# Kernel tuning notes

Hardware: AMD Instinct MI355X
Metric: run time of the kernel (lower is better)

Reference implementation:

```python
import jax, jax.numpy as jnp
import numpy as np

N_NODES = 10000
N_EDGES = 320000
F_IN = 128
HID = 32


def sage_mean(x, src, dst, W_self, W_neigh, b, n_nodes):
    # mean aggregation over in-neighbors (messages flow src -> dst)
    msg = x[src]                                   # [E, F]
    agg = jax.ops.segment_sum(msg, dst, num_segments=n_nodes)   # [N, F]
    deg = jax.ops.segment_sum(jnp.ones((src.shape[0],), x.dtype), dst,
                              num_segments=n_nodes)             # [N]
    h_neigh = agg / jnp.maximum(deg, 1.0)[:, None]
    return x @ W_self + h_neigh @ W_neigh + b


def setup_inputs() -> dict:
    key = jax.random.key(0)
    ks = jax.random.split(key, 12)
    s = 0.05
    return {
        "n_feats": jax.random.normal(ks[0], (N_NODES, F_IN), jnp.float32),
        "src": jax.random.randint(ks[1], (N_EDGES,), 0, N_NODES, jnp.int32),
        "dst": jax.random.randint(ks[2], (N_EDGES,), 0, N_NODES, jnp.int32),
        "eps": jax.random.normal(ks[3], (N_NODES, HID), jnp.float32),
        "W1_self": jax.random.normal(ks[4], (F_IN, HID), jnp.float32) * s,
        "W1_neigh": jax.random.normal(ks[5], (F_IN, HID), jnp.float32) * s,
        "b1": jnp.zeros((HID,), jnp.float32),
        "Wmu_self": jax.random.normal(ks[6], (HID, HID), jnp.float32) * s,
        "Wmu_neigh": jax.random.normal(ks[7], (HID, HID), jnp.float32) * s,
        "bmu": jnp.zeros((HID,), jnp.float32),
        "Wls_self": jax.random.normal(ks[8], (HID, HID), jnp.float32) * s,
        "Wls_neigh": jax.random.normal(ks[9], (HID, HID), jnp.float32) * s,
        "bls": jnp.zeros((HID,), jnp.float32),
    }


def reference(n_feats, src, dst, eps, W1_self, W1_neigh, b1,
              Wmu_self, Wmu_neigh, bmu, Wls_self, Wls_neigh, bls):
    n = n_feats.shape[0]
    h = jax.nn.relu(sage_mean(n_feats, src, dst, W1_self, W1_neigh, b1, n))
    mu = sage_mean(h, src, dst, Wmu_self, Wmu_neigh, bmu, n)
    logstd = sage_mean(h, src, dst, Wls_self, Wls_neigh, bls, n)
    z = mu + eps * jnp.exp(logstd)          # reparameterize
    adj = jax.nn.sigmoid(z @ z.T)           # dot-product decode, [N, N]
    return adj, mu, logstd
```

## Files before the change

kernel.cpp:

```cpp
#include <hip/hip_runtime.h>
#include <hip/hip_bf16.h>


#define N_NODES 10000
#define N_EDGES 320000
#define F_IN 128
#define HID 32

__global__ __launch_bounds__(256) void k_gemm_in(
    const float* __restrict__ x, const float* __restrict__ Ws,
    const float* __restrict__ Wn, const float* __restrict__ b,
    float* __restrict__ outS, float* __restrict__ outN) {
  __shared__ float sWs[F_IN * HID];
  __shared__ float sWn[F_IN * HID];
  __shared__ float sx[32 * F_IN];
  const int t = threadIdx.x;
  const int node0 = blockIdx.x * 32;
  #pragma unroll
  for (int i = t * 4; i < F_IN * HID; i += 1024) {
    *(float4*)&sWs[i] = *(const float4*)&Ws[i];
    *(float4*)&sWn[i] = *(const float4*)&Wn[i];
  }
  #pragma unroll
  for (int i = t * 4; i < 32 * F_IN; i += 1024) {
    const int r = i >> 7, k = i & 127;
    const int gr = node0 + r;
    float4 v = make_float4(0.f, 0.f, 0.f, 0.f);
    if (gr < N_NODES) v = *(const float4*)&x[gr * F_IN + k];
    *(float4*)&sx[i] = v;
  }
  __syncthreads();
  const int c = t & 31, g = t >> 5;
  float accS[4] = {0.f, 0.f, 0.f, 0.f};
  float accN[4] = {0.f, 0.f, 0.f, 0.f};
  #pragma unroll 4
  for (int k = 0; k < F_IN; ++k) {
    const float ws = sWs[k * HID + c];
    const float wn = sWn[k * HID + c];
    #pragma unroll
    for (int m = 0; m < 4; ++m) {
      const float a = sx[(g + 8 * m) * F_IN + k];
      accS[m] += a * ws;
      accN[m] += a * wn;
    }
  }
  const float bc = b[c];
  #pragma unroll
  for (int m = 0; m < 4; ++m) {
    const int node = node0 + g + 8 * m;
    if (node < N_NODES) {
      outS[node * HID + c] = accS[m] + bc;
      outN[node * HID + c] = accN[m];
    }
  }
}

__global__ __launch_bounds__(256) void k_aggregate(
    const float* __restrict__ feat, const int* __restrict__ src,
    const int* __restrict__ dst, float* __restrict__ agg,
    float* __restrict__ deg) {
  const int tid = blockIdx.x * 256 + threadIdx.x;
  const int e = tid >> 5;
  const int k = tid & 31;
  if (e >= N_EDGES) return;
  const int s = src[e];
  const int d = dst[e];
  atomicAdd(&agg[d * HID + k], feat[s * HID + k]);
  if (deg != nullptr && k == 0) atomicAdd(&deg[d], 1.0f);
}

__global__ __launch_bounds__(256) void k_layer1_finish(
    const float* __restrict__ xws, const float* __restrict__ agg,
    const float* __restrict__ deg, float* __restrict__ h) {
  const int i = blockIdx.x * 256 + threadIdx.x;
  if (i >= N_NODES * HID) return;
  const int node = i >> 5;
  float dv = deg[node];
  dv = dv > 1.f ? dv : 1.f;
  const float v = xws[i] + agg[i] / dv;
  h[i] = v > 0.f ? v : 0.f;
}

__global__ __launch_bounds__(256) void k_layer2(
    const float* __restrict__ h, const float* __restrict__ aggh,
    const float* __restrict__ deg, const float* __restrict__ eps,
    const float* __restrict__ Wms, const float* __restrict__ Wmn,
    const float* __restrict__ bm, const float* __restrict__ Wls,
    const float* __restrict__ Wln, const float* __restrict__ bl,
    float* __restrict__ mu_out, float* __restrict__ ls_out,
    float* __restrict__ z) {
  __shared__ float sMs[HID * HID], sMn[HID * HID];
  __shared__ float sLs[HID * HID], sLn[HID * HID];
  __shared__ float sh[8 * HID], shn[8 * HID];
  const int t = threadIdx.x;
  {
    const int i = t * 4;
    *(float4*)&sMs[i] = *(const float4*)&Wms[i];
    *(float4*)&sMn[i] = *(const float4*)&Wmn[i];
    *(float4*)&sLs[i] = *(const float4*)&Wls[i];
    *(float4*)&sLn[i] = *(const float4*)&Wln[i];
  }
  const int node0 = blockIdx.x * 8;
  const int lr = t >> 5;
  const int gnode_ld = node0 + lr;
  if (gnode_ld < N_NODES) {
    float dv = deg[gnode_ld];
    dv = dv > 1.f ? dv : 1.f;
    sh[t] = h[node0 * HID + t];
    shn[t] = aggh[node0 * HID + t] / dv;
  } else {
    sh[t] = 0.f;
    shn[t] = 0.f;
  }
  __syncthreads();
  const int r = t >> 5, c = t & 31;
  const int node = node0 + r;
  float mu = 0.f, ls = 0.f;
  #pragma unroll 8
  for (int k = 0; k < HID; ++k) {
    const float a = sh[r * HID + k];
    const float an = shn[r * HID + k];
    mu += a * sMs[k * HID + c] + an * sMn[k * HID + c];
    ls += a * sLs[k * HID + c] + an * sLn[k * HID + c];
  }
  if (node < N_NODES) {
    mu += bm[c];
    ls += bl[c];
    const int idx = node * HID + c;
    mu_out[idx] = mu;
    ls_out[idx] = ls;
    z[idx] = mu + eps[idx] * __expf(ls);
  }
}

#define NT_COL 157
#define NWG (NT_COL * NT_COL)
#define NWG_Q (NWG / 8)
#define NWG_R (NWG % 8)
__global__ __launch_bounds__(256, 4) void k_decode(const float* __restrict__ z,
                                                   float* __restrict__ adj) {
  __shared__ float za[64][36];
  __shared__ float zb[64][36];
  const int bid = blockIdx.x;
  const int xcd = bid & 7, idx = bid >> 3;
  const int wg = (xcd < NWG_R) ? xcd * (NWG_Q + 1) + idx
                               : NWG_R * (NWG_Q + 1) + (xcd - NWG_R) * NWG_Q + idx;
  const int rowt = wg / NT_COL, colt = wg % NT_COL;
  const int r0 = rowt * 64;
  const int c0 = colt * 64;
  const int t = threadIdx.x;
  #pragma unroll
  for (int i = t; i < 512; i += 256) {
    const int row = i >> 3, k4 = (i & 7) << 2;
    const int gr = r0 + row;
    const int gc = c0 + row;
    float4 va = make_float4(0.f, 0.f, 0.f, 0.f);
    float4 vb = make_float4(0.f, 0.f, 0.f, 0.f);
    if (gr < N_NODES) va = *(const float4*)&z[gr * HID + k4];
    if (gc < N_NODES) vb = *(const float4*)&z[gc * HID + k4];
    *(float4*)&za[row][k4] = va;
    *(float4*)&zb[row][k4] = vb;
  }
  __syncthreads();
  const int tx = t & 15, ty = t >> 4;
  float acc[4][4];
  #pragma unroll
  for (int i = 0; i < 4; ++i)
    #pragma unroll
    for (int j = 0; j < 4; ++j) acc[i][j] = 0.f;

  #pragma unroll 4
  for (int k = 0; k < HID; ++k) {
    float a[4], b[4];
    #pragma unroll
    for (int i = 0; i < 4; ++i) a[i] = za[ty + i * 16][k];
    #pragma unroll
    for (int j = 0; j < 4; ++j) b[j] = zb[tx + j * 16][k];
    #pragma unroll
    for (int i = 0; i < 4; ++i)
      #pragma unroll
      for (int j = 0; j < 4; ++j) acc[i][j] += a[i] * b[j];
  }

  #pragma unroll
  for (int i = 0; i < 4; ++i) {
    const int r = r0 + ty + i * 16;
    if (r >= N_NODES) continue;
    float* rowp = adj + (size_t)r * N_NODES;
    #pragma unroll
    for (int j = 0; j < 4; ++j) {
      const int c = c0 + tx + j * 16;
      if (c < N_NODES) {
        const float v = acc[i][j];
        rowp[c] = __builtin_amdgcn_rcpf(1.f + __expf(-v));
      }
    }
  }
}

extern "C" void kernel_launch(void* const* d_in, const int* in_sizes, int n_in,
                              void* d_out, int out_size, void* d_ws,
                              size_t ws_size, hipStream_t stream) {
  const float* x   = (const float*)d_in[0];
  const int* src   = (const int*)d_in[1];
  const int* dst   = (const int*)d_in[2];
  const float* eps = (const float*)d_in[3];
  const float* W1s = (const float*)d_in[4];
  const float* W1n = (const float*)d_in[5];
  const float* b1  = (const float*)d_in[6];
  const float* Wms = (const float*)d_in[7];
  const float* Wmn = (const float*)d_in[8];
  const float* bm  = (const float*)d_in[9];
  const float* Wls = (const float*)d_in[10];
  const float* Wln = (const float*)d_in[11];
  const float* bl  = (const float*)d_in[12];

  float* out = (float*)d_out;
  float* adj = out;
  float* mu_out = out + (size_t)N_NODES * N_NODES;
  float* ls_out = mu_out + (size_t)N_NODES * HID;

  float* ws = (float*)d_ws;
  float* deg  = ws;
  float* agg  = ws + N_NODES;
  float* aggh = agg + N_NODES * HID;
  float* xws  = aggh + N_NODES * HID;
  float* xwn  = xws + N_NODES * HID;
  float* h    = xwn + N_NODES * HID;
  float* z    = h + N_NODES * HID;
  (void)ws_size; (void)in_sizes; (void)n_in; (void)out_size;

  hipMemsetAsync(ws, 0, (size_t)(N_NODES + 2 * N_NODES * HID) * sizeof(float),
                 stream);

  k_gemm_in<<<dim3((N_NODES + 31) / 32), dim3(256), 0, stream>>>(
      x, W1s, W1n, b1, xws, xwn);
  k_aggregate<<<dim3((N_EDGES * HID) / 256), dim3(256), 0, stream>>>(
      xwn, src, dst, agg, deg);
  k_layer1_finish<<<dim3((N_NODES * HID) / 256), dim3(256), 0, stream>>>(
      xws, agg, deg, h);
  k_aggregate<<<dim3((N_EDGES * HID) / 256), dim3(256), 0, stream>>>(
      h, src, dst, aggh, nullptr);
  k_layer2<<<dim3((N_NODES + 7) / 8), dim3(256), 0, stream>>>(
      h, aggh, deg, eps, Wms, Wmn, bm, Wls, Wln, bl, mu_out, ls_out, z);
  k_decode<<<dim3(NWG), dim3(256), 0, stream>>>(z, adj);
}
```

Baseline: 578.3 us.

## Use split-bf16 MFMA with 128x128 tiles for the dot-product decode

The z·zᵀ decode now splits each fp32 value into high and low bf16 halves and computes the product with three bf16 MFMA 16x16x32 ops per tile (hi·hi, hi·lo, lo·hi), replacing the scalar FMA loop. Tiles grow from 64x64 to 128x128, each wave handling a 64x64 quadrant. Interior tiles skip the per-element bounds checks. The kernel is dominated by writing the 400MB adj output, so the gain is limited to the compute share. The store pattern changes to column-strided per lane, and the low-order cross term is dropped, which gives slightly lower precision than fp32.

```diff
diff --git a/kernel.cpp b/kernel.cpp
--- a/kernel.cpp
+++ b/kernel.cpp
@@ -6,6 +6,9 @@
 #define N_EDGES 320000
 #define F_IN 128
 #define HID 32
+
+typedef short bf16x8 __attribute__((ext_vector_type(8)));
+typedef float f32x4 __attribute__((ext_vector_type(4)));
 
 __global__ __launch_bounds__(256) void k_gemm_in(
     const float* __restrict__ x, const float* __restrict__ Ws,
@@ -133,66 +136,101 @@
   }
 }
 
-#define NT_COL 157
-#define NWG (NT_COL * NT_COL)
-#define NWG_Q (NWG / 8)
-#define NWG_R (NWG % 8)
-__global__ __launch_bounds__(256, 4) void k_decode(const float* __restrict__ z,
-                                                   float* __restrict__ adj) {
-  __shared__ float za[64][36];
-  __shared__ float zb[64][36];
+#define NT 79
+#define DNWG (NT * NT)
+#define DNWG_Q (DNWG / 8)
+#define DNWG_R (DNWG % 8)
+#define ROWP 40
+
+__global__ __launch_bounds__(256) void k_decode(const float* __restrict__ z,
+                                                float* __restrict__ adj) {
+  __shared__ short sah[128 * ROWP];
+  __shared__ short sal[128 * ROWP];
+  __shared__ short sbh[128 * ROWP];
+  __shared__ short sbl[128 * ROWP];
+
   const int bid = blockIdx.x;
   const int xcd = bid & 7, idx = bid >> 3;
-  const int wg = (xcd < NWG_R) ? xcd * (NWG_Q + 1) + idx
-                               : NWG_R * (NWG_Q + 1) + (xcd - NWG_R) * NWG_Q + idx;
-  const int rowt = wg / NT_COL, colt = wg % NT_COL;
-  const int r0 = rowt * 64;
-  const int c0 = colt * 64;
+  const int wg = (xcd < DNWG_R)
+                     ? xcd * (DNWG_Q + 1) + idx
+                     : DNWG_R * (DNWG_Q + 1) + (xcd - DNWG_R) * DNWG_Q + idx;
+  const int r0 = (wg / NT) * 128;
+  const int c0 = (wg % NT) * 128;
   const int t = threadIdx.x;
-  #pragma unroll
-  for (int i = t; i < 512; i += 256) {
-    const int row = i >> 3, k4 = (i & 7) << 2;
-    const int gr = r0 + row;
-    const int gc = c0 + row;
+
+  for (int i = t; i < 1024; i += 256) {
+    const int row = i >> 3;
+    const int kq = (i & 7) << 2;
+    const int gr = r0 + row, gc = c0 + row;
     float4 va = make_float4(0.f, 0.f, 0.f, 0.f);
     float4 vb = make_float4(0.f, 0.f, 0.f, 0.f);
-    if (gr < N_NODES) va = *(const float4*)&z[gr * HID + k4];
-    if (gc < N_NODES) vb = *(const float4*)&z[gc * HID + k4];
-    *(float4*)&za[row][k4] = va;
-    *(float4*)&zb[row][k4] = vb;
+    if (gr < N_NODES) va = *(const float4*)&z[gr * HID + kq];
+    if (gc < N_NODES) vb = *(const float4*)&z[gc * HID + kq];
+    const float fa[4] = {va.x, va.y, va.z, va.w};
+    const float fb[4] = {vb.x, vb.y, vb.z, vb.w};
+    short ha[4], la[4], hb[4], lb[4];
+    #pragma unroll
+    for (int e = 0; e < 4; ++e) {
+      unsigned ua = __float_as_uint(fa[e]);
+      ha[e] = (short)(ua >> 16);
+      float ra = fa[e] - __uint_as_float(ua & 0xFFFF0000u);
+      la[e] = (short)(__float_as_uint(ra) >> 16);
+      unsigned ub = __float_as_uint(fb[e]);
+      hb[e] = (short)(ub >> 16);
+      float rb = fb[e] - __uint_as_float(ub & 0xFFFF0000u);
+      lb[e] = (short)(__float_as_uint(rb) >> 16);
+    }
+    const int off = row * ROWP + kq;
+    *(short4*)&sah[off] = make_short4(ha[0], ha[1], ha[2], ha[3]);
+    *(short4*)&sal[off] = make_short4(la[0], la[1], la[2], la[3]);
+    *(short4*)&sbh[off] = make_short4(hb[0], hb[1], hb[2], hb[3]);
+    *(short4*)&sbl[off] = make_short4(lb[0], lb[1], lb[2], lb[3]);
   }
   __syncthreads();
-  const int tx = t & 15, ty = t >> 4;
-  float acc[4][4];
-  #pragma unroll
-  for (int i = 0; i < 4; ++i)
-    #pragma unroll
-    for (int j = 0; j < 4; ++j) acc[i][j] = 0.f;
-
-  #pragma unroll 4
-  for (int k = 0; k < HID; ++k) {
-    float a[4], b[4];
-    #pragma unroll
-    for (int i = 0; i < 4; ++i) a[i] = za[ty + i * 16][k];
-    #pragma unroll
-    for (int j = 0; j < 4; ++j) b[j] = zb[tx + j * 16][k];
-    #pragma unroll
-    for (int i = 0; i < 4; ++i)
-      #pragma unroll
-      for (int j = 0; j < 4; ++j) acc[i][j] += a[i] * b[j];
+
+  const int wid = t >> 6;
+  const int lane = t & 63;
+  const int wr = (wid >> 1) * 64;
+  const int wc = (wid & 1) * 64;
+  const int lrow = lane & 15;
+  const int lchunk = lane >> 4;
+  const bool interior = (r0 + 128 <= N_NODES) && (c0 + 128 <= N_NODES);
+
+  bf16x8 Bh[4], Bl[4];
+  #pragma unroll
+  for (int j = 0; j < 4; ++j) {
+    const int boff = (wc + j * 16 + lrow) * ROWP + lchunk * 8;
+    Bh[j] = *(const bf16x8*)&sbh[boff];
+    Bl[j] = *(const bf16x8*)&sbl[boff];
   }
 
   #pragma unroll
   for (int i = 0; i < 4; ++i) {
-    const int r = r0 + ty + i * 16;
-    if (r >= N_NODES) continue;
-    float* rowp = adj + (size_t)r * N_NODES;
+    const int aoff = (wr + i * 16 + lrow) * ROWP + lchunk * 8;
+    const bf16x8 Ah = *(const bf16x8*)&sah[aoff];
+    const bf16x8 Al = *(const bf16x8*)&sal[aoff];
     #pragma unroll
     for (int j = 0; j < 4; ++j) {
-      const int c = c0 + tx + j * 16;
-      if (c < N_NODES) {
-        const float v = acc[i][j];
-        rowp[c] = __builtin_amdgcn_rcpf(1.f + __expf(-v));
+      f32x4 acc = {0.f, 0.f, 0.f, 0.f};
+      acc = __builtin_amdgcn_mfma_f32_16x16x32_bf16(Ah, Bh[j], acc, 0, 0, 0);
+      acc = __builtin_amdgcn_mfma_f32_16x16x32_bf16(Ah, Bl[j], acc, 0, 0, 0);
+      acc = __builtin_amdgcn_mfma_f32_16x16x32_bf16(Al, Bh[j], acc, 0, 0, 0);
+      const int ccol = c0 + wc + j * 16 + lrow;
+      const int rbase = r0 + wr + i * 16 + lchunk * 4;
+      if (interior) {
+        #pragma unroll
+        for (int r = 0; r < 4; ++r) {
+          const float s = __builtin_amdgcn_rcpf(1.f + __expf(-acc[r]));
+          adj[(size_t)(rbase + r) * N_NODES + ccol] = s;
+        }
+      } else {
+        #pragma unroll
+        for (int r = 0; r < 4; ++r) {
+          if (rbase + r < N_NODES && ccol < N_NODES) {
+            const float s = __builtin_amdgcn_rcpf(1.f + __expf(-acc[r]));
+            adj[(size_t)(rbase + r) * N_NODES + ccol] = s;
+          }
+        }
       }
     }
   }
@@ -243,5 +281,5 @@
       h, src, dst, aggh, nullptr);
   k_layer2<<<dim3((N_NODES + 7) / 8), dim3(256), 0, stream>>>(
       h, aggh, deg, eps, Wms, Wmn, bm, Wls, Wln, bl, mu_out, ls_out, z);
-  k_decode<<<dim3(NWG), dim3(256), 0, stream>>>(z, adj);
-}
+  k_decode<<<dim3(DNWG), dim3(256), 0, stream>>>(z, adj);
+}
```

Result: faster. 555.9 us (-3.9%).
